# Kernel tuning notes

Measured on AMD Instinct MI355X. Metric: run time of the kernel, lower is better.

The kernel has to match this reference:

```python
import jax, jax.numpy as jnp
import numpy as np

N, E, F_IN, C = 50000, 800000, 128, 300
NEG_SLOPE = 0.2  # PyG GATv2Conv default negative_slope


def setup_inputs() -> dict:
    key = jax.random.key(0)
    ks = jax.random.split(key, 10)
    x = jax.random.normal(ks[0], (N, F_IN), dtype=jnp.float32)
    edge_index = jax.random.randint(ks[1], (2, E), 0, N, dtype=jnp.int64)
    s_in = np.float32(1.0 / np.sqrt(F_IN))
    s_c = np.float32(1.0 / np.sqrt(C))
    Wl = jax.random.normal(ks[2], (F_IN, C), dtype=jnp.float32) * s_in
    bl = jnp.zeros((C,), jnp.float32)
    Wr = jax.random.normal(ks[3], (F_IN, C), dtype=jnp.float32) * s_in
    br = jnp.zeros((C,), jnp.float32)
    att = jax.random.normal(ks[4], (C,), dtype=jnp.float32) * s_c
    bias = jnp.zeros((C,), jnp.float32)
    lw = jax.random.normal(ks[5], (C, 1), dtype=jnp.float32) * s_c
    lb = jnp.zeros((1,), jnp.float32)
    return {"x": x, "edge_index": edge_index, "Wl": Wl, "bl": bl,
            "Wr": Wr, "br": br, "att": att, "bias": bias, "lw": lw, "lb": lb}


def reference(x, edge_index, Wl, bl, Wr, br, att, bias, lw, lb):
    n = x.shape[0]
    # GATv2: separate source/target linear transforms
    xl = x @ Wl + bl  # [N, C] (source / message features)
    xr = x @ Wr + br  # [N, C] (target features)
    # add self loops (PyG default add_self_loops=True)
    loops = jnp.arange(n, dtype=edge_index.dtype)
    src = jnp.concatenate([edge_index[0], loops])  # [E+N]
    dst = jnp.concatenate([edge_index[1], loops])  # [E+N]
    # GATv2 attention logit: a^T LeakyReLU(xl_j + xr_i)
    e = jax.nn.leaky_relu(xl[src] + xr[dst], NEG_SLOPE) @ att  # [E+N]
    # segment softmax over incoming edges of each target node
    m = jax.ops.segment_max(e, dst, num_segments=n)
    ex = jnp.exp(e - m[dst])
    denom = jax.ops.segment_sum(ex, dst, num_segments=n)
    alpha = ex / denom[dst]  # [E+N]
    # weighted scatter-aggregation of source messages + conv bias
    out = jax.ops.segment_sum(xl[src] * alpha[:, None], dst, num_segments=n) + bias
    h = jax.nn.relu(out)          # torch.relu
    # F.dropout in eval mode is identity (reference is inference math)
    return jax.nn.sigmoid(h @ lw + lb)  # [N, 1]
```

## Files before the change

### kernel.cpp

```cpp
#include <hip/hip_runtime.h>
#include <hip/hip_fp16.h>

#define F_IN 128
#define C_DIM 300
#define NEG_SLOPE 0.2f
#define NCT  38
#define CTH  19
#define CH   8
#define NPB  256

typedef _Float16 half8 __attribute__((ext_vector_type(8)));
typedef _Float16 half4 __attribute__((ext_vector_type(4)));
typedef _Float16 h2    __attribute__((ext_vector_type(2)));
typedef float    f32x4 __attribute__((ext_vector_type(4)));
typedef float    f32x2 __attribute__((ext_vector_type(2)));

__device__ inline h2 as_h2(unsigned u) { union { unsigned u; h2 h; } c; c.u = u; return c.h; }
__device__ inline unsigned as_u(h2 h)  { union { unsigned u; h2 h; } c; c.h = h; return c.u; }
__device__ inline f32x2 upv(unsigned u) {
    h2 h = as_h2(u);
    f32x2 r; r.x = (float)h.x; r.y = (float)h.y; return r;
}

#if __has_builtin(__builtin_amdgcn_fdot2)
__device__ inline float fdot2w(h2 a, h2 b, float c) {
    return __builtin_amdgcn_fdot2(a, b, c, false);
}
#else
__device__ inline float fdot2w(h2 a, h2 b, float c) {
    return fmaf((float)a.y, (float)b.y, fmaf((float)a.x, (float)b.x, c));
}
#endif

__global__ __launch_bounds__(256) void convert_w(
    const float* __restrict__ Wl, const float* __restrict__ Wr,
    _Float16* __restrict__ Bp)
{
    int idx = blockIdx.x * 256 + threadIdx.x;
    if (idx >= 608 * F_IN) return;
    int nn = idx % 608;
    int k  = idx / 608;
    float v = 0.f;
    if (nn < 300)                   v = Wl[k * C_DIM + nn];
    else if (nn >= 304 && nn < 604) v = Wr[k * C_DIM + (nn - 304)];
    int ct = nn >> 4, n16 = nn & 15;
    int kr = k & 31,  ks  = k >> 5;
    int lane = ((kr >> 3) << 4) | n16;
    int j = k & 7;
    Bp[((((ct * 4 + ks) * 64) + lane) << 3) | j] = (_Float16)v;
}

__global__ __launch_bounds__(256) void gemm_xlxr(
    const float* __restrict__ x, const _Float16* __restrict__ Bp,
    const float* __restrict__ bl, const float* __restrict__ br,
    _Float16* __restrict__ xlh, _Float16* __restrict__ xrh, int n)
{
    __shared__ __align__(16) _Float16 xs[64][136];
    const int rg  = blockIdx.x >> 1;
    const int cs  = blockIdx.x & 1;
    const int rb0 = rg * 64;
    const int t   = threadIdx.x;

    #pragma unroll
    for (int i = 0; i < 8; ++i) {
        int flat = (i * 256 + t) * 4;
        int r = flat >> 7;
        int k = flat & 127;
        int gr = rb0 + r;
        if (gr >= n) gr = n - 1;
        float4 v = *reinterpret_cast<const float4*>(x + (size_t)gr * F_IN + k);
        half4 h = { (_Float16)v.x, (_Float16)v.y, (_Float16)v.z, (_Float16)v.w };
        *reinterpret_cast<half4*>(&xs[r][k]) = h;
    }
    __syncthreads();

    const int w    = t >> 6;
    const int lane = t & 63;
    const int m    = lane & 15;
    const int quad = lane >> 4;

    half8 a[4];
    #pragma unroll
    for (int ks = 0; ks < 4; ++ks)
        a[ks] = *reinterpret_cast<const half8*>(&xs[w * 16 + m][ks * 32 + quad * 8]);

    const int rbase = rb0 + w * 16 + quad * 4;
    const int ct0   = cs * CTH;

    const half8* bp = reinterpret_cast<const half8*>(Bp) ;
    half8 bc0 = bp[((size_t)(ct0 * 4 + 0) * 64) + lane];
    half8 bc1 = bp[((size_t)(ct0 * 4 + 1) * 64) + lane];
    half8 bc2 = bp[((size_t)(ct0 * 4 + 2) * 64) + lane];
    half8 bc3 = bp[((size_t)(ct0 * 4 + 3) * 64) + lane];

    for (int ci = 0; ci < CTH; ++ci) {
        const int ct  = ct0 + ci;
        const int ctn = (ci < CTH - 1) ? ct + 1 : ct;
        half8 bn0 = bp[((size_t)(ctn * 4 + 0) * 64) + lane];
        half8 bn1 = bp[((size_t)(ctn * 4 + 1) * 64) + lane];
        half8 bn2 = bp[((size_t)(ctn * 4 + 2) * 64) + lane];
        half8 bn3 = bp[((size_t)(ctn * 4 + 3) * 64) + lane];

        f32x4 acc = {0.f, 0.f, 0.f, 0.f};
        acc = __builtin_amdgcn_mfma_f32_16x16x32_f16(a[0], bc0, acc, 0, 0, 0);
        acc = __builtin_amdgcn_mfma_f32_16x16x32_f16(a[1], bc1, acc, 0, 0, 0);
        acc = __builtin_amdgcn_mfma_f32_16x16x32_f16(a[2], bc2, acc, 0, 0, 0);
        acc = __builtin_amdgcn_mfma_f32_16x16x32_f16(a[3], bc3, acc, 0, 0, 0);

        int col = ct * 16 + m;
        int isL = (col < 300);
        int isR = (col >= 304 && col < 604);
        if (isL | isR) {
            float bv = isL ? bl[col] : br[col - 304];
            _Float16* tab = isL ? (xlh + col) : (xrh + (col - 304));
            #pragma unroll
            for (int reg = 0; reg < 4; ++reg) {
                int row = rbase + reg;
                if (row < n)
                    tab[(size_t)row * C_DIM] = (_Float16)(acc[reg] + bv);
            }
        }
        bc0 = bn0; bc1 = bn1; bc2 = bn2; bc3 = bn3;
    }
}

__global__ __launch_bounds__(256) void bucket_count(
    const int* __restrict__ dst, unsigned* __restrict__ bcnt, int nE, int chunk4)
{
    __shared__ unsigned cnt[256];
    const int b = blockIdx.x, t = threadIdx.x;
    cnt[t] = 0;
    __syncthreads();
    const int4* dst4 = reinterpret_cast<const int4*>(dst);
    const int total4 = (nE + 3) >> 2;
    const int lo = b * chunk4;
    const int hi = min(total4, lo + chunk4);
    for (int i = lo + t; i < hi; i += 256) {
        int4 d = dst4[i];
        int e = i * 4;
        if (e + 3 < nE) {
            atomicAdd(&cnt[d.x >> 8], 1u);
            atomicAdd(&cnt[d.y >> 8], 1u);
            atomicAdd(&cnt[d.z >> 8], 1u);
            atomicAdd(&cnt[d.w >> 8], 1u);
        } else {
            if (e < nE)     atomicAdd(&cnt[d.x >> 8], 1u);
            if (e + 1 < nE) atomicAdd(&cnt[d.y >> 8], 1u);
            if (e + 2 < nE) atomicAdd(&cnt[d.z >> 8], 1u);
        }
    }
    __syncthreads();
    bcnt[t * NPB + b] = cnt[t];
}

__global__ __launch_bounds__(256) void scan_part(
    const unsigned* __restrict__ counts, unsigned* __restrict__ bsum, int n)
{
    __shared__ unsigned s[256];
    const int t = threadIdx.x;
    const int base = blockIdx.x * 1024 + t * 4;
    unsigned v = 0;
    #pragma unroll
    for (int i = 0; i < 4; ++i) {
        int idx = base + i;
        if (idx < n) v += counts[idx];
    }
    s[t] = v;
    __syncthreads();
    for (int off = 128; off > 0; off >>= 1) {
        if (t < off) s[t] += s[t + off];
        __syncthreads();
    }
    if (t == 0) bsum[blockIdx.x] = s[0];
}

__global__ __launch_bounds__(256) void scan_final(
    const unsigned* __restrict__ counts, const unsigned* __restrict__ bsum,
    unsigned* __restrict__ offs, int n, int nblk)
{
    __shared__ unsigned s[256];
    __shared__ unsigned sbase;
    const int t = threadIdx.x;
    if (t < 64) {
        unsigned v64 = (t < nblk) ? bsum[t] : 0u;
        unsigned inc = v64;
        #pragma unroll
        for (int off = 1; off < 64; off <<= 1) {
            unsigned u = __shfl_up(inc, off);
            if (t >= off) inc += u;
        }
        if (t == (int)blockIdx.x) sbase = inc - v64;
        if (blockIdx.x == gridDim.x - 1 && t == 63) offs[n] = inc;
    }
    const int base = blockIdx.x * 1024 + t * 4;
    unsigned c[4];
    unsigned v = 0;
    #pragma unroll
    for (int i = 0; i < 4; ++i) {
        int idx = base + i;
        c[i] = (idx < n) ? counts[idx] : 0u;
        v += c[i];
    }
    s[t] = v;
    __syncthreads();
    for (int off = 1; off < 256; off <<= 1) {
        unsigned u = (t >= off) ? s[t - off] : 0u;
        __syncthreads();
        if (t >= off) s[t] += u;
        __syncthreads();
    }
    unsigned run = sbase + s[t] - v;
    #pragma unroll
    for (int i = 0; i < 4; ++i) {
        int idx = base + i;
        if (idx < n) {
            offs[idx] = run;
            run += c[i];
        }
    }
}

__global__ __launch_bounds__(256) void partition_edges(
    const int* __restrict__ src, const int* __restrict__ dst,
    const unsigned* __restrict__ boff,
    unsigned* __restrict__ ebuf, int nE, int chunk4)
{
    __shared__ unsigned cur[256];
    const int b = blockIdx.x, t = threadIdx.x;
    cur[t] = boff[t * NPB + b];
    __syncthreads();
    const int4* dst4 = reinterpret_cast<const int4*>(dst);
    const int4* src4 = reinterpret_cast<const int4*>(src);
    const int total4 = (nE + 3) >> 2;
    const int lo = b * chunk4;
    const int hi = min(total4, lo + chunk4);
    for (int i = lo + t; i < hi; i += 256) {
        int4 d = dst4[i];
        int4 s = src4[i];
        int e = i * 4;
        int dv[4] = {d.x, d.y, d.z, d.w};
        int sv[4] = {s.x, s.y, s.z, s.w};
        #pragma unroll
        for (int j = 0; j < 4; ++j) {
            if (e + j < nE) {
                unsigned p = atomicAdd(&cur[dv[j] >> 8], 1u);
                ebuf[p] = (unsigned)sv[j] | ((unsigned)(dv[j] & 255) << 16);
            }
        }
    }
}

__global__ __launch_bounds__(256) void bucket_csr(
    const unsigned* __restrict__ ebuf, const unsigned* __restrict__ boff,
    unsigned* __restrict__ offs, int* __restrict__ csr_src, int n, int nE, int nb)
{
    __shared__ unsigned cnt[256];
    __shared__ unsigned s[256];
    __shared__ unsigned cur[256];
    const int bk = blockIdx.x;
    const int t  = threadIdx.x;
    const unsigned bstart = boff[(unsigned)bk * NPB];
    const unsigned bend   = boff[(unsigned)(bk + 1) * NPB];
    cnt[t] = 0;
    __syncthreads();
    for (unsigned i = bstart + t; i < bend; i += 256)
        atomicAdd(&cnt[(ebuf[i] >> 16) & 255], 1u);
    __syncthreads();
    unsigned v = cnt[t];
    s[t] = v;
    __syncthreads();
    for (int off = 1; off < 256; off <<= 1) {
        unsigned u = (t >= off) ? s[t - off] : 0u;
        __syncthreads();
        if (t >= off) s[t] += u;
        __syncthreads();
    }
    const unsigned excl = s[t] - v;
    const int node = (bk << 8) + t;
    if (node <= n) offs[node] = bstart + excl;
    if (t == 0 && bk == nb - 1 && (n & 255) == 0) offs[n] = (unsigned)nE;
    cur[t] = bstart + excl;
    __syncthreads();
    for (unsigned i = bstart + t; i < bend; i += 256) {
        unsigned e = ebuf[i];
        unsigned p = atomicAdd(&cur[(e >> 16) & 255], 1u);
        csr_src[p] = (int)(e & 0xFFFFu);
    }
}

__global__ __launch_bounds__(256) void gat_gather(
    const int* __restrict__ csr_src, const unsigned* __restrict__ offs,
    const _Float16* __restrict__ xlh, const _Float16* __restrict__ xrh,
    const float* __restrict__ att, const float* __restrict__ bias,
    const float* __restrict__ lw, const float* __restrict__ lb,
    float* __restrict__ y, int n)
{
    __shared__ __align__(16) float lds[4 * 560];
    float* part = lds + (threadIdx.x >> 6) * 560;

    const int wid  = (blockIdx.x * blockDim.x + threadIdx.x) >> 6;
    const int lane = threadIdx.x & 63;
    if (wid >= n) return;

    const int l2   = 2 * lane;
    const bool has2 = (lane < 22);
    const int t8   = lane & 7;
    const int o    = lane >> 3;
    const int byteoff = lane * 4;

    const _Float16* xrrow = xrh + (size_t)wid * C_DIM;
    h2 xr0 = *(const h2*)(xrrow + l2);
    h2 xr1 = *(const h2*)(xrrow + 128 + l2);
    h2 xr2 = {(_Float16)0, (_Float16)0};
    if (has2) xr2 = *(const h2*)(xrrow + 256 + l2);

    h2 a06[3], a04[3];
    #pragma unroll
    for (int k = 0; k < 3; ++k) {
        int c = 128 * k + l2;
        float ax = (c < C_DIM) ? att[c] : 0.f;
        float ay = (c + 1 < C_DIM) ? att[c + 1] : 0.f;
        a06[k].x = (_Float16)(0.6f * ax); a06[k].y = (_Float16)(0.6f * ay);
        a04[k].x = (_Float16)(0.4f * ax); a04[k].y = (_Float16)(0.4f * ay);
    }

    f32x2 acc2[3] = {{0.f, 0.f}, {0.f, 0.f}, {0.f, 0.f}};
    float den_l = 0.f;

    const unsigned start = offs[wid];
    const int totalE = (int)(offs[wid + 1] - start) + 1;
    const char* basep = (const char*)xlh;

    int idv = wid;
    {
        int k = lane;
        if (lane < CH && k > 0 && k < totalE) idv = csr_src[start + k - 1];
    }

    for (int base = 0; base < totalE; base += CH) {
        int rowb = idv * (C_DIM * 2);
        int ro[CH];
        #pragma unroll
        for (int tt = 0; tt < CH; ++tt) ro[tt] = __shfl(rowb, tt);

        unsigned pk0[CH], pk1[CH], pk2[CH];
        #pragma unroll
        for (int tt = 0; tt < CH; ++tt) {
            const char* p = basep + ro[tt] + byteoff;
            pk0[tt] = *(const unsigned*)(p);
            pk1[tt] = *(const unsigned*)(p + 256);
            pk2[tt] = 0u;
        }
        if (has2) {
            #pragma unroll
            for (int tt = 0; tt < CH; ++tt)
                pk2[tt] = *(const unsigned*)(basep + ro[tt] + byteoff + 512);
        }

        idv = wid;
        {
            int k = base + CH + lane;
            if (lane < CH && k > 0 && k < totalE) idv = csr_src[start + k - 1];
        }

        #pragma unroll
        for (int tt = 0; tt < CH; ++tt) {
            h2 z0 = as_h2(pk0[tt]) + xr0;
            h2 z1 = as_h2(pk1[tt]) + xr1;
            h2 z2 = as_h2(pk2[tt]) + xr2;
            float p = fdot2w(z0, a06[0], 0.f);
            p = fdot2w(as_h2(as_u(z0) & 0x7FFF7FFFu), a04[0], p);
            p = fdot2w(z1, a06[1], p);
            p = fdot2w(as_h2(as_u(z1) & 0x7FFF7FFFu), a04[1], p);
            p = fdot2w(z2, a06[2], p);
            p = fdot2w(as_h2(as_u(z2) & 0x7FFF7FFFu), a04[2], p);
            part[tt * 68 + lane] = p;
        }

        float wgt;
        {
            const int oo = (o + t8) & 7;
            const float* rp = part + t8 * 68 + oo * 8;
            float4 s0 = *(const float4*)(rp + 0);
            float4 s1 = *(const float4*)(rp + 4);
            float e = ((s0.x + s0.y) + (s0.z + s0.w)) + ((s1.x + s1.y) + (s1.z + s1.w));
            e += __shfl_xor(e, 8);
            e += __shfl_xor(e, 16);
            e += __shfl_xor(e, 32);
            bool valid = (base + t8) < totalE;
            wgt = valid ? __expf(fminf(e, 60.f)) : 0.f;
        }

        den_l += wgt;

        _Float16 wh = (_Float16)wgt;
        h2 wpair = {wh, wh};
        unsigned wbits = as_u(wpair);
        h2 hacc0 = {(_Float16)0, (_Float16)0};
        h2 hacc1 = {(_Float16)0, (_Float16)0};
        h2 hacc2 = {(_Float16)0, (_Float16)0};
        #pragma unroll
        for (int tt = 0; tt < CH; ++tt) {
            h2 wt2 = as_h2(__shfl(wbits, tt));
            hacc0 += wt2 * as_h2(pk0[tt]);
            hacc1 += wt2 * as_h2(pk1[tt]);
            hacc2 += wt2 * as_h2(pk2[tt]);
        }
        acc2[0] += upv(as_u(hacc0));
        acc2[1] += upv(as_u(hacc1));
        acc2[2] += upv(as_u(hacc2));
    }

    float den = den_l;
    den += __shfl_xor(den, 1);
    den += __shfl_xor(den, 2);
    den += __shfl_xor(den, 4);

    const float invd = 1.f / den;
    float dot = 0.f;
    #pragma unroll
    for (int k = 0; k < 3; ++k) {
        #pragma unroll
        for (int j = 0; j < 2; ++j) {
            int c = 128 * k + l2 + j;
            float b = (c < C_DIM) ? bias[c] : 0.f;
            float l = (c < C_DIM) ? lw[c] : 0.f;
            float a = (j == 0) ? acc2[k].x : acc2[k].y;
            float h = fmaf(a, invd, b);
            h = h > 0.f ? h : 0.f;
            dot = fmaf(h, l, dot);
        }
    }
    #pragma unroll
    for (int off = 32; off; off >>= 1) dot += __shfl_xor(dot, off);
    if (lane == 0) y[wid] = 1.f / (1.f + __expf(-(dot + lb[0])));
}

extern "C" void kernel_launch(void* const* d_in, const int* in_sizes, int n_in,
                              void* d_out, int out_size, void* d_ws, size_t ws_size,
                              hipStream_t stream)
{
    const float* x    = (const float*)d_in[0];
    const int*   ei   = (const int*)d_in[1];
    const float* Wl   = (const float*)d_in[2];
    const float* bl   = (const float*)d_in[3];
    const float* Wr   = (const float*)d_in[4];
    const float* br   = (const float*)d_in[5];
    const float* att  = (const float*)d_in[6];
    const float* bias = (const float*)d_in[7];
    const float* lw   = (const float*)d_in[8];
    const float* lb   = (const float*)d_in[9];
    float* y = (float*)d_out;

    const int n  = in_sizes[0] / F_IN;
    const int nE = in_sizes[1] / 2;
    const int* src_arr = ei;
    const int* dst_arr = ei + nE;

    const int NB     = (n + 255) >> 8;
    const int total4 = (nE + 3) >> 2;
    const int chunk4 = (total4 + NPB - 1) / NPB;
    const int M      = 256 * NPB;
    const int nblkM  = (M + 1023) / 1024;

    _Float16* xlh      = (_Float16*)d_ws;
    _Float16* xrh      = xlh + (size_t)n * C_DIM;
    _Float16* Bp       = xrh + (size_t)n * C_DIM;
    unsigned* bcnt     = (unsigned*)(Bp + NCT * 4 * 64 * 8);
    unsigned* boff     = bcnt + M;
    unsigned* offs     = boff + (M + 1);
    unsigned* bsum     = offs + (n + 1);
    int*      csr_src  = (int*)(bsum + 64);
    unsigned* ebuf     = (unsigned*)(csr_src + nE);

    convert_w<<<(608 * F_IN + 255) / 256, 256, 0, stream>>>(Wl, Wr, Bp);

    bucket_count<<<NPB, 256, 0, stream>>>(dst_arr, bcnt, nE, chunk4);
    scan_part<<<nblkM, 256, 0, stream>>>(bcnt, bsum, M);
    scan_final<<<nblkM, 256, 0, stream>>>(bcnt, bsum, boff, M, nblkM);
    partition_edges<<<NPB, 256, 0, stream>>>(src_arr, dst_arr, boff, ebuf, nE, chunk4);
    bucket_csr<<<NB, 256, 0, stream>>>(ebuf, boff, offs, csr_src, n, nE, NB);

    gemm_xlxr<<<((n + 63) / 64) * 2, 256, 0, stream>>>(x, Bp, bl, br, xlh, xrh, n);

    gat_gather<<<(n + 3) / 4, 256, 0, stream>>>(csr_src, offs, xlh, xrh, att, bias, lw, lb, y, n);
}
```

Measured before the change: 229.9 us.

## Fuse weight convert and CSR build into one persistent kernel with grid barriers

Merges the weight repack, bucket count, two-level scan, edge partition and per-bucket CSR kernels into a single 256-block kernel. The stages are separated by a software grid barrier built on an atomic counter, which is reset by a memset before each launch. The scan is restructured as a row scan, then a row-sum scan, across the block/bucket matrix. The aim is to remove several kernel launches and the inter-kernel gaps. In exchange, correctness depends on all 256 blocks being co-resident, and the spin-wait barriers add their own cost.

Result: slower. 380.5 us (+65.5%).

```diff
diff --git a/kernel.cpp b/kernel.cpp
--- a/kernel.cpp
+++ b/kernel.cpp
@@ -32,22 +32,161 @@
 }
 #endif
 
-__global__ __launch_bounds__(256) void convert_w(
+__device__ inline void gbar(unsigned* ctr, unsigned k)
+{
+    __threadfence();
+    __syncthreads();
+    if (threadIdx.x == 0) {
+        atomicAdd(ctr, 1u);
+        const unsigned target = NPB * k;
+        while (__hip_atomic_load(ctr, __ATOMIC_RELAXED, __HIP_MEMORY_SCOPE_AGENT) < target) {
+#if __has_builtin(__builtin_amdgcn_s_sleep)
+            __builtin_amdgcn_s_sleep(8);
+#endif
+        }
+        __threadfence();
+    }
+    __syncthreads();
+}
+
+__global__ __launch_bounds__(256) void csr_fused(
     const float* __restrict__ Wl, const float* __restrict__ Wr,
-    _Float16* __restrict__ Bp)
+    _Float16* __restrict__ Bp,
+    const int* __restrict__ src, const int* __restrict__ dst,
+    unsigned* __restrict__ bcnt, unsigned* __restrict__ boff,
+    unsigned* __restrict__ rowsum, unsigned* __restrict__ ebuf,
+    unsigned* __restrict__ offs, int* __restrict__ csr_src,
+    unsigned* __restrict__ ctr, int n, int nE, int chunk4)
 {
-    int idx = blockIdx.x * 256 + threadIdx.x;
-    if (idx >= 608 * F_IN) return;
-    int nn = idx % 608;
-    int k  = idx / 608;
-    float v = 0.f;
-    if (nn < 300)                   v = Wl[k * C_DIM + nn];
-    else if (nn >= 304 && nn < 604) v = Wr[k * C_DIM + (nn - 304)];
-    int ct = nn >> 4, n16 = nn & 15;
-    int kr = k & 31,  ks  = k >> 5;
-    int lane = ((kr >> 3) << 4) | n16;
-    int j = k & 7;
-    Bp[((((ct * 4 + ks) * 64) + lane) << 3) | j] = (_Float16)v;
+    __shared__ unsigned cnt[256];
+    __shared__ unsigned s[256];
+    __shared__ unsigned cur[256];
+    const int b = blockIdx.x;
+    const int t = threadIdx.x;
+
+    for (int idx = b * 256 + t; idx < 608 * F_IN; idx += NPB * 256) {
+        int nn = idx % 608;
+        int k  = idx / 608;
+        float v = 0.f;
+        if (nn < 300)                   v = Wl[k * C_DIM + nn];
+        else if (nn >= 304 && nn < 604) v = Wr[k * C_DIM + (nn - 304)];
+        int ct = nn >> 4, n16 = nn & 15;
+        int kr = k & 31,  ks  = k >> 5;
+        int lane = ((kr >> 3) << 4) | n16;
+        int j = k & 7;
+        Bp[((((ct * 4 + ks) * 64) + lane) << 3) | j] = (_Float16)v;
+    }
+
+    cnt[t] = 0;
+    __syncthreads();
+    {
+        const int4* dst4 = reinterpret_cast<const int4*>(dst);
+        const int total4 = (nE + 3) >> 2;
+        const int lo = b * chunk4;
+        const int hi = min(total4, lo + chunk4);
+        for (int i = lo + t; i < hi; i += 256) {
+            int4 d = dst4[i];
+            int e = i * 4;
+            if (e + 3 < nE) {
+                atomicAdd(&cnt[d.x >> 8], 1u);
+                atomicAdd(&cnt[d.y >> 8], 1u);
+                atomicAdd(&cnt[d.z >> 8], 1u);
+                atomicAdd(&cnt[d.w >> 8], 1u);
+            } else {
+                if (e < nE)     atomicAdd(&cnt[d.x >> 8], 1u);
+                if (e + 1 < nE) atomicAdd(&cnt[d.y >> 8], 1u);
+                if (e + 2 < nE) atomicAdd(&cnt[d.z >> 8], 1u);
+            }
+        }
+    }
+    __syncthreads();
+    bcnt[t * NPB + b] = cnt[t];
+
+    gbar(ctr, 1);
+
+    unsigned c0 = bcnt[b * 256 + t];
+    s[t] = c0;
+    __syncthreads();
+    for (int off = 1; off < 256; off <<= 1) {
+        unsigned u = (t >= off) ? s[t - off] : 0u;
+        __syncthreads();
+        if (t >= off) s[t] += u;
+        __syncthreads();
+    }
+    const unsigned rexcl = s[t] - c0;
+    if (t == 255) rowsum[b] = s[255];
+
+    gbar(ctr, 2);
+
+    unsigned rs = rowsum[t];
+    s[t] = rs;
+    __syncthreads();
+    for (int off = 1; off < 256; off <<= 1) {
+        unsigned u = (t >= off) ? s[t - off] : 0u;
+        __syncthreads();
+        if (t >= off) s[t] += u;
+        __syncthreads();
+    }
+    const unsigned rowbase = (b > 0) ? s[b - 1] : 0u;
+    boff[b * 256 + t] = rowbase + rexcl;
+
+    gbar(ctr, 3);
+
+    cur[t] = boff[t * NPB + b];
+    __syncthreads();
+    {
+        const int4* dst4 = reinterpret_cast<const int4*>(dst);
+        const int4* src4 = reinterpret_cast<const int4*>(src);
+        const int total4 = (nE + 3) >> 2;
+        const int lo = b * chunk4;
+        const int hi = min(total4, lo + chunk4);
+        for (int i = lo + t; i < hi; i += 256) {
+            int4 d = dst4[i];
+            int4 sv4 = src4[i];
+            int e = i * 4;
+            int dv[4] = {d.x, d.y, d.z, d.w};
+            int sv[4] = {sv4.x, sv4.y, sv4.z, sv4.w};
+            #pragma unroll
+            for (int j = 0; j < 4; ++j) {
+                if (e + j < nE) {
+                    unsigned p = atomicAdd(&cur[dv[j] >> 8], 1u);
+                    ebuf[p] = (unsigned)sv[j] | ((unsigned)(dv[j] & 255) << 16);
+                }
+            }
+        }
+    }
+
+    gbar(ctr, 4);
+
+    const int nb = (n + 255) >> 8;
+    if (b >= nb) return;
+    const unsigned bstart = boff[(unsigned)b * NPB];
+    const unsigned bend   = boff[(unsigned)(b + 1) * NPB];
+    cnt[t] = 0;
+    __syncthreads();
+    for (unsigned i = bstart + t; i < bend; i += 256)
+        atomicAdd(&cnt[(ebuf[i] >> 16) & 255], 1u);
+    __syncthreads();
+    unsigned v = cnt[t];
+    s[t] = v;
+    __syncthreads();
+    for (int off = 1; off < 256; off <<= 1) {
+        unsigned u = (t >= off) ? s[t - off] : 0u;
+        __syncthreads();
+        if (t >= off) s[t] += u;
+        __syncthreads();
+    }
+    const unsigned excl = s[t] - v;
+    const int node = (b << 8) + t;
+    if (node <= n) offs[node] = bstart + excl;
+    if (t == 0 && b == nb - 1 && (n & 255) == 0) offs[n] = (unsigned)nE;
+    cur[t] = bstart + excl;
+    __syncthreads();
+    for (unsigned i = bstart + t; i < bend; i += 256) {
+        unsigned e = ebuf[i];
+        unsigned p = atomicAdd(&cur[(e >> 16) & 255], 1u);
+        csr_src[p] = (int)(e & 0xFFFFu);
+    }
 }
 
 __global__ __launch_bounds__(256) void gemm_xlxr(
@@ -87,7 +226,7 @@
     const int rbase = rb0 + w * 16 + quad * 4;
     const int ct0   = cs * CTH;
 
-    const half8* bp = reinterpret_cast<const half8*>(Bp) ;
+    const half8* bp = reinterpret_cast<const half8*>(Bp);
     half8 bc0 = bp[((size_t)(ct0 * 4 + 0) * 64) + lane];
     half8 bc1 = bp[((size_t)(ct0 * 4 + 1) * 64) + lane];
     half8 bc2 = bp[((size_t)(ct0 * 4 + 2) * 64) + lane];
@@ -121,170 +260,6 @@
             }
         }
         bc0 = bn0; bc1 = bn1; bc2 = bn2; bc3 = bn3;
-    }
-}
-
-__global__ __launch_bounds__(256) void bucket_count(
-    const int* __restrict__ dst, unsigned* __restrict__ bcnt, int nE, int chunk4)
-{
-    __shared__ unsigned cnt[256];
-    const int b = blockIdx.x, t = threadIdx.x;
-    cnt[t] = 0;
-    __syncthreads();
-    const int4* dst4 = reinterpret_cast<const int4*>(dst);
-    const int total4 = (nE + 3) >> 2;
-    const int lo = b * chunk4;
-    const int hi = min(total4, lo + chunk4);
-    for (int i = lo + t; i < hi; i += 256) {
-        int4 d = dst4[i];
-        int e = i * 4;
-        if (e + 3 < nE) {
-            atomicAdd(&cnt[d.x >> 8], 1u);
-            atomicAdd(&cnt[d.y >> 8], 1u);
-            atomicAdd(&cnt[d.z >> 8], 1u);
-            atomicAdd(&cnt[d.w >> 8], 1u);
-        } else {
-            if (e < nE)     atomicAdd(&cnt[d.x >> 8], 1u);
-            if (e + 1 < nE) atomicAdd(&cnt[d.y >> 8], 1u);
-            if (e + 2 < nE) atomicAdd(&cnt[d.z >> 8], 1u);
-        }
-    }
-    __syncthreads();
-    bcnt[t * NPB + b] = cnt[t];
-}
-
-__global__ __launch_bounds__(256) void scan_part(
-    const unsigned* __restrict__ counts, unsigned* __restrict__ bsum, int n)
-{
-    __shared__ unsigned s[256];
-    const int t = threadIdx.x;
-    const int base = blockIdx.x * 1024 + t * 4;
-    unsigned v = 0;
-    #pragma unroll
-    for (int i = 0; i < 4; ++i) {
-        int idx = base + i;
-        if (idx < n) v += counts[idx];
-    }
-    s[t] = v;
-    __syncthreads();
-    for (int off = 128; off > 0; off >>= 1) {
-        if (t < off) s[t] += s[t + off];
-        __syncthreads();
-    }
-    if (t == 0) bsum[blockIdx.x] = s[0];
-}
-
-__global__ __launch_bounds__(256) void scan_final(
-    const unsigned* __restrict__ counts, const unsigned* __restrict__ bsum,
-    unsigned* __restrict__ offs, int n, int nblk)
-{
-    __shared__ unsigned s[256];
-    __shared__ unsigned sbase;
-    const int t = threadIdx.x;
-    if (t < 64) {
-        unsigned v64 = (t < nblk) ? bsum[t] : 0u;
-        unsigned inc = v64;
-        #pragma unroll
-        for (int off = 1; off < 64; off <<= 1) {
-            unsigned u = __shfl_up(inc, off);
-            if (t >= off) inc += u;
-        }
-        if (t == (int)blockIdx.x) sbase = inc - v64;
-        if (blockIdx.x == gridDim.x - 1 && t == 63) offs[n] = inc;
-    }
-    const int base = blockIdx.x * 1024 + t * 4;
-    unsigned c[4];
-    unsigned v = 0;
-    #pragma unroll
-    for (int i = 0; i < 4; ++i) {
-        int idx = base + i;
-        c[i] = (idx < n) ? counts[idx] : 0u;
-        v += c[i];
-    }
-    s[t] = v;
-    __syncthreads();
-    for (int off = 1; off < 256; off <<= 1) {
-        unsigned u = (t >= off) ? s[t - off] : 0u;
-        __syncthreads();
-        if (t >= off) s[t] += u;
-        __syncthreads();
-    }
-    unsigned run = sbase + s[t] - v;
-    #pragma unroll
-    for (int i = 0; i < 4; ++i) {
-        int idx = base + i;
-        if (idx < n) {
-            offs[idx] = run;
-            run += c[i];
-        }
-    }
-}
-
-__global__ __launch_bounds__(256) void partition_edges(
-    const int* __restrict__ src, const int* __restrict__ dst,
-    const unsigned* __restrict__ boff,
-    unsigned* __restrict__ ebuf, int nE, int chunk4)
-{
-    __shared__ unsigned cur[256];
-    const int b = blockIdx.x, t = threadIdx.x;
-    cur[t] = boff[t * NPB + b];
-    __syncthreads();
-    const int4* dst4 = reinterpret_cast<const int4*>(dst);
-    const int4* src4 = reinterpret_cast<const int4*>(src);
-    const int total4 = (nE + 3) >> 2;
-    const int lo = b * chunk4;
-    const int hi = min(total4, lo + chunk4);
-    for (int i = lo + t; i < hi; i += 256) {
-        int4 d = dst4[i];
-        int4 s = src4[i];
-        int e = i * 4;
-        int dv[4] = {d.x, d.y, d.z, d.w};
-        int sv[4] = {s.x, s.y, s.z, s.w};
-        #pragma unroll
-        for (int j = 0; j < 4; ++j) {
-            if (e + j < nE) {
-                unsigned p = atomicAdd(&cur[dv[j] >> 8], 1u);
-                ebuf[p] = (unsigned)sv[j] | ((unsigned)(dv[j] & 255) << 16);
-            }
-        }
-    }
-}
-
-__global__ __launch_bounds__(256) void bucket_csr(
-    const unsigned* __restrict__ ebuf, const unsigned* __restrict__ boff,
-    unsigned* __restrict__ offs, int* __restrict__ csr_src, int n, int nE, int nb)
-{
-    __shared__ unsigned cnt[256];
-    __shared__ unsigned s[256];
-    __shared__ unsigned cur[256];
-    const int bk = blockIdx.x;
-    const int t  = threadIdx.x;
-    const unsigned bstart = boff[(unsigned)bk * NPB];
-    const unsigned bend   = boff[(unsigned)(bk + 1) * NPB];
-    cnt[t] = 0;
-    __syncthreads();
-    for (unsigned i = bstart + t; i < bend; i += 256)
-        atomicAdd(&cnt[(ebuf[i] >> 16) & 255], 1u);
-    __syncthreads();
-    unsigned v = cnt[t];
-    s[t] = v;
-    __syncthreads();
-    for (int off = 1; off < 256; off <<= 1) {
-        unsigned u = (t >= off) ? s[t - off] : 0u;
-        __syncthreads();
-        if (t >= off) s[t] += u;
-        __syncthreads();
-    }
-    const unsigned excl = s[t] - v;
-    const int node = (bk << 8) + t;
-    if (node <= n) offs[node] = bstart + excl;
-    if (t == 0 && bk == nb - 1 && (n & 255) == 0) offs[n] = (unsigned)nE;
-    cur[t] = bstart + excl;
-    __syncthreads();
-    for (unsigned i = bstart + t; i < bend; i += 256) {
-        unsigned e = ebuf[i];
-        unsigned p = atomicAdd(&cur[(e >> 16) & 255], 1u);
-        csr_src[p] = (int)(e & 0xFFFFu);
     }
 }
 
@@ -457,11 +432,9 @@
     const int* src_arr = ei;
     const int* dst_arr = ei + nE;
 
-    const int NB     = (n + 255) >> 8;
     const int total4 = (nE + 3) >> 2;
     const int chunk4 = (total4 + NPB - 1) / NPB;
     const int M      = 256 * NPB;
-    const int nblkM  = (M + 1023) / 1024;
 
     _Float16* xlh      = (_Float16*)d_ws;
     _Float16* xrh      = xlh + (size_t)n * C_DIM;
@@ -469,17 +442,16 @@
     unsigned* bcnt     = (unsigned*)(Bp + NCT * 4 * 64 * 8);
     unsigned* boff     = bcnt + M;
     unsigned* offs     = boff + (M + 1);
-    unsigned* bsum     = offs + (n + 1);
-    int*      csr_src  = (int*)(bsum + 64);
+    unsigned* rowsum   = offs + (n + 1);
+    unsigned* ctr      = rowsum + 256;
+    int*      csr_src  = (int*)(ctr + 8);
     unsigned* ebuf     = (unsigned*)(csr_src + nE);
 
-    convert_w<<<(608 * F_IN + 255) / 256, 256, 0, stream>>>(Wl, Wr, Bp);
-
-    bucket_count<<<NPB, 256, 0, stream>>>(dst_arr, bcnt, nE, chunk4);
-    scan_part<<<nblkM, 256, 0, stream>>>(bcnt, bsum, M);
-    scan_final<<<nblkM, 256, 0, stream>>>(bcnt, bsum, boff, M, nblkM);
-    partition_edges<<<NPB, 256, 0, stream>>>(src_arr, dst_arr, boff, ebuf, nE, chunk4);
-    bucket_csr<<<NB, 256, 0, stream>>>(ebuf, boff, offs, csr_src, n, nE, NB);
+    hipMemsetAsync(ctr, 0, 4, stream);
+
+    csr_fused<<<NPB, 256, 0, stream>>>(Wl, Wr, Bp, src_arr, dst_arr,
+                                       bcnt, boff, rowsum, ebuf, offs, csr_src,
+                                       ctr, n, nE, chunk4);
 
     gemm_xlxr<<<((n + 63) / 64) * 2, 256, 0, stream>>>(x, Bp, bl, br, xlh, xrh, n);
 
```
